# Optimization experiments

Hardware: AMD Instinct MI355X
Metric: run time of the kernel (lower is better)

Reference implementation:

```python
import jax, jax.numpy as jnp
import numpy as np

T, K, H, I, E = 8192, 2, 1024, 2816, 8


def setup_inputs() -> dict:
    key = jax.random.key(0)
    k1, k2, k3, k4, k5 = jax.random.split(key, 5)
    hidden_states = jax.random.normal(k1, (T, H), dtype=jnp.float32)
    expert_routing_table = jax.random.randint(k2, (T, K), 0, E)
    router_weights = jax.random.uniform(k3, (T, K), dtype=jnp.float32)
    # permuted_weights=True: weights stored so forward is x @ w
    # w13: fused gate+up proj [E, H, 2I]; w2: down proj [E, I, H]
    w13 = jax.random.normal(k4, (E, H, 2 * I), dtype=jnp.float32) * (1.0 / np.sqrt(H))
    w2 = jax.random.normal(k5, (E, I, H), dtype=jnp.float32) * (1.0 / np.sqrt(I))
    return {
        "hidden_states": hidden_states,
        "expert_routing_table": expert_routing_table,
        "router_weights": router_weights,
        "w13": w13,
        "w2": w2,
    }


def reference(hidden_states, expert_routing_table, router_weights, w13, w2):
    # Semantics of hpu.mixture_of_experts with activation='silu':
    # out[t] = sum_k rw[t,k] * ( (silu(x@w1g[e]) * (x@w1u[e])) @ w2[e] ), e = table[t,k]
    n_experts = w13.shape[0]
    inter = w2.shape[1]
    # per-token combine coefficient for each expert: [T, E]
    onehot = jax.nn.one_hot(expert_routing_table, n_experts, dtype=hidden_states.dtype)  # [T,K,E]
    coeff = jnp.einsum("tke,tk->te", onehot, router_weights)
    out = jnp.zeros_like(hidden_states)
    for e in range(n_experts):
        gu = hidden_states @ w13[e]            # [T, 2I]
        gate, up = gu[:, :inter], gu[:, inter:]
        h = jax.nn.silu(gate) * up             # [T, I]
        out = out + coeff[:, e:e + 1] * (h @ w2[e])
    return out
```

## Files before the change

kernel.cpp:

```cpp
#include <hip/hip_runtime.h>

typedef unsigned short u16;
typedef unsigned int u32;
typedef __bf16 bf16x8 __attribute__((ext_vector_type(8)));
typedef float f32x4 __attribute__((ext_vector_type(4)));
typedef u16 u16x4 __attribute__((ext_vector_type(4)));
typedef u16 u16x8 __attribute__((ext_vector_type(8)));

#define T_TOK 8192
#define HDIM 1024
#define IDIM 2816
#define NEXP 8
#define NPAIR (T_TOK * 2)
#define MAXRB 71

#define XB_OFF   (147456u)
#define W13T_OFF (XB_OFF + 16777216u)
#define W2T_OFF  (W13T_OFF + 92274688u)
#define H_OFF    (W2T_OFF + 46137344u)
#define WS_NEED  ((size_t)H_OFF + 102367232u)

__device__ __forceinline__ u16 f2bf(float f) {
  u32 u = __builtin_bit_cast(u32, f);
  u32 r = u + 0x7fffu + ((u >> 16) & 1u);
  return (u16)(r >> 16);
}

#define GLD16(g, l) __builtin_amdgcn_global_load_lds( \
    (const __attribute__((address_space(1))) void*)(g), \
    (__attribute__((address_space(3))) void*)(l), 16, 0, 0)

#define WAITVM(N) asm volatile("s_waitcnt vmcnt(" #N ")" ::: "memory")

__device__ __forceinline__ void pbar() {
  __builtin_amdgcn_sched_barrier(0);
  asm volatile("" ::: "memory");
  __builtin_amdgcn_s_barrier();
  asm volatile("" ::: "memory");
  __builtin_amdgcn_sched_barrier(0);
}

__global__ void init_meta(int* meta) {
  if (threadIdx.x < 16) meta[threadIdx.x] = 0;
}

__global__ void count_k(const int* __restrict__ routing, int* __restrict__ meta) {
  int i = blockIdx.x * 256 + threadIdx.x;
  if (i < NPAIR) atomicAdd(&meta[routing[i]], 1);
}

__global__ void scan_k(int* __restrict__ meta) {
  if (threadIdx.x == 0) {
    int rb = 0;
    for (int e = 0; e < NEXP; ++e) {
      meta[16 + e] = rb * 256;
      int nrb = (meta[e] + 255) >> 8;
      for (int i = 0; i < nrb; ++i) meta[32 + rb + i] = e;
      rb += nrb;
    }
    meta[24] = rb;
  }
}

__global__ void fill_pairs(int* __restrict__ pairs) {
  pairs[blockIdx.x * 256 + threadIdx.x] = -1;
}

__global__ void scatter_k(const int* __restrict__ routing, int* __restrict__ meta,
                          int* __restrict__ pairs, int* __restrict__ inv) {
  int i = blockIdx.x * 256 + threadIdx.x;
  if (i < NPAIR) {
    int e = routing[i];
    int pos = atomicAdd(&meta[8 + e], 1);
    int row = meta[16 + e] + pos;
    pairs[row] = i;
    inv[i] = row;
  }
}

__global__ void conv_x(const float* __restrict__ in, u16* __restrict__ out) {
  int i = blockIdx.x * 256 + threadIdx.x;
  float4 a = ((const float4*)in)[2 * i];
  float4 b = ((const float4*)in)[2 * i + 1];
  u16x8 o = { f2bf(a.x), f2bf(a.y), f2bf(a.z), f2bf(a.w),
              f2bf(b.x), f2bf(b.y), f2bf(b.z), f2bf(b.w) };
  ((u16x8*)out)[i] = o;
}

#define TSW(r, c) (((((c) >> 2) ^ ((((r) >> 4) & 3) << 2)) << 2) | ((c) & 3))
__global__ void transpose_cvt(const float* __restrict__ in, u16* __restrict__ out,
                              int R, int C) {
  __shared__ float tile[64][68];
  size_t base = (size_t)blockIdx.z * (size_t)R * (size_t)C;
  in += base; out += base;
  int t = threadIdx.x;
  int r0 = blockIdx.y * 64, c0 = blockIdx.x * 64;
  int lr = t >> 4, cb = t & 15;
#pragma unroll
  for (int p = 0; p < 4; ++p) {
    int row = p * 16 + lr;
    float4 v = *(const float4*)&in[(size_t)(r0 + row) * C + c0 + cb * 4];
    int pc = ((cb ^ ((p & 3) << 2)) << 2);
    tile[row][pc] = v.x; tile[row][pc + 1] = v.y;
    tile[row][pc + 2] = v.z; tile[row][pc + 3] = v.w;
  }
  __syncthreads();
  int oc = t >> 2, g0 = (t & 3) * 2;
#pragma unroll
  for (int gg = 0; gg < 2; ++gg) {
    int g = g0 + gg;
    u16x8 o = { f2bf(tile[g * 8 + 0][TSW(g * 8 + 0, oc)]), f2bf(tile[g * 8 + 1][TSW(g * 8 + 1, oc)]),
                f2bf(tile[g * 8 + 2][TSW(g * 8 + 2, oc)]), f2bf(tile[g * 8 + 3][TSW(g * 8 + 3, oc)]),
                f2bf(tile[g * 8 + 4][TSW(g * 8 + 4, oc)]), f2bf(tile[g * 8 + 5][TSW(g * 8 + 5, oc)]),
                f2bf(tile[g * 8 + 6][TSW(g * 8 + 6, oc)]), f2bf(tile[g * 8 + 7][TSW(g * 8 + 7, oc)]) };
    *(u16x8*)&out[(size_t)(c0 + oc) * R + r0 + g * 8] = o;
  }
}

__global__ __launch_bounds__(512, 2) void gemm1_k(
    const u16* __restrict__ Xb, const u16* __restrict__ W13T,
    const int* __restrict__ pairs, const int* __restrict__ meta,
    const float* __restrict__ rwf, u16* __restrict__ Hb) {
  int lin = blockIdx.x + 22 * blockIdx.y;
  int xcd = lin & 7, slot = lin >> 3;
  int flat = (xcd < 2) ? xcd * 196 + slot : 392 + (xcd - 2) * 195 + slot;
  int bx = flat / 71, rb = flat % 71;
  if (rb >= meta[24]) return;
  const int e = meta[32 + rb];
  const int bn0 = bx * 128;
  const int tid = threadIdx.x, lane = tid & 63, w = tid >> 6;
  const int wr = w >> 2, wc = w & 3;
  const int rowBase = rb * 256;

  __shared__ __align__(16) u16 lds[65536];
  char* const lb = (char*)lds;

  const int tr = tid >> 3;
  const int swk = ((tid & 7) << 4) ^ ((tr & 7) << 4);
  const u16* aS[4]; const u16* bS[4];
  const u16* wBase = W13T + (size_t)e * (2 * IDIM) * HDIM;
#pragma unroll
  for (int s = 0; s < 4; ++s) {
    int pr = pairs[rowBase + s * 64 + tr];
    int tok = pr < 0 ? 0 : (pr >> 1);
    aS[s] = Xb + (size_t)tok * HDIM + (swk >> 1);
    bS[s] = wBase + (size_t)((tr >> 5) * IDIM + bn0 + s * 32 + (tr & 31)) * HDIM + (swk >> 1);
  }

#define STGA(b, h, kt) { GLD16(aS[(h)*2]   + (kt)*64, lb + (b)*32768 + (h)*16384 + tid*16); \
                         GLD16(aS[(h)*2+1] + (kt)*64, lb + (b)*32768 + (h)*16384 + 8192 + tid*16); }
#define STGB(b, h, kt) { GLD16(bS[(h)*2]   + (kt)*64, lb + 65536 + (b)*32768 + (h)*16384 + tid*16); \
                         GLD16(bS[(h)*2+1] + (kt)*64, lb + 65536 + (b)*32768 + (h)*16384 + 8192 + tid*16); }

  const int l15 = lane & 15, l4 = lane >> 4, l7 = lane & 7;
  const int ko0 = (l4 * 16) ^ (l7 << 4);
  const int ko1 = (64 + l4 * 16) ^ (l7 << 4);
  const int aFB = wr * 16384 + l15 * 128;
  const int bFB = 65536 + (wc * 64 + l15) * 128;

#define LDA(d, b, mh, mf, ko) d = *(const bf16x8*)(lb + (b)*32768 + aFB + (mh)*8192 + (mf)*2048 + (ko))
#define LDB(d, b, nf, ko)     d = *(const bf16x8*)(lb + (b)*32768 + bFB + (nf)*2048 + (ko))

#define MFQ(mh, A, B) \
  _Pragma("unroll") for (int mf = 0; mf < 4; ++mf) \
  _Pragma("unroll") for (int nf = 0; nf < 4; ++nf) \
    acc[(mh)*4+mf][nf] = __builtin_amdgcn_mfma_f32_16x16x32_bf16(A[mf], B[nf], acc[(mh)*4+mf][nf], 0, 0, 0);

  f32x4 acc[8][4];
  const f32x4 fz = {0.f, 0.f, 0.f, 0.f};
#pragma unroll
  for (int i = 0; i < 8; ++i)
#pragma unroll
    for (int j = 0; j < 4; ++j) acc[i][j] = fz;

  STGB(0, 0, 0); STGB(0, 1, 0); STGA(0, 0, 0); STGA(0, 1, 0); STGB(1, 0, 1); STGB(1, 1, 1);
  WAITVM(4);
  pbar();

  bf16x8 aF[4], b0F[4], b1F[4];
#define ITER1(b, t1, t2) { \
     \
    _Pragma("unroll") for (int f = 0; f < 4; ++f) { LDA(aF[f], b, 0, f, ko0); LDB(b0F[f], b, f, ko0); } \
    STGA((b)^1, 0, t1); \
    pbar(); \
    __builtin_amdgcn_s_setprio(1); MFQ(0, aF, b0F); __builtin_amdgcn_s_setprio(0); \
    pbar(); \
     \
    _Pragma("unroll") for (int f = 0; f < 4; ++f) { LDA(aF[f], b, 0, f, ko1); LDB(b1F[f], b, f, ko1); } \
    STGA((b)^1, 1, t1); \
    pbar(); \
    __builtin_amdgcn_s_setprio(1); MFQ(0, aF, b1F); __builtin_amdgcn_s_setprio(0); \
    pbar(); \
     \
    _Pragma("unroll") for (int f = 0; f < 4; ++f) { LDA(aF[f], b, 1, f, ko0); } \
    STGB(b, 0, t2); \
    pbar(); \
    __builtin_amdgcn_s_setprio(1); MFQ(1, aF, b0F); __builtin_amdgcn_s_setprio(0); \
    pbar(); \
     \
    _Pragma("unroll") for (int f = 0; f < 4; ++f) { LDA(aF[f], b, 1, f, ko1); } \
    STGB(b, 1, t2); \
    pbar(); \
    __builtin_amdgcn_s_setprio(1); MFQ(1, aF, b1F); __builtin_amdgcn_s_setprio(0); \
    WAITVM(4); \
    pbar(); \
  }

  for (int jj = 0; jj < 8; ++jj) {
    const int ta = (2 * jj + 1) & 15, tb = (2 * jj + 2) & 15, tc = (2 * jj + 3) & 15;
    ITER1(0, ta, tb);
    ITER1(1, tb, tc);
  }
#undef ITER1
#undef STGA
#undef STGB
#undef LDA
#undef LDB
#undef MFQ

  const int ct = l4;
#pragma unroll
  for (int mf = 0; mf < 8; ++mf) {
#pragma unroll
    for (int j = 0; j < 4; ++j) {
      int m = wr * 128 + mf * 16 + ct * 4 + j;
      int pr = rowBase + m;
      int pair = pairs[pr];
      float rw = pair >= 0 ? rwf[pair] : 0.f;
      u16* hrow = Hb + (size_t)pr * IDIM + bn0 + wc * 32 + l15;
#pragma unroll
      for (int g = 0; g < 2; ++g) {
        float gv = acc[mf][g][j], uv = acc[mf][g + 2][j];
        float s = gv / (1.f + __expf(-gv));
        hrow[g * 16] = f2bf(s * uv * rw);
      }
    }
  }
}

__global__ __launch_bounds__(256, 2) void gemm2_k(
    const u16* __restrict__ Hb, const u16* __restrict__ W2T,
    const int* __restrict__ meta, float* __restrict__ part) {
  int lin = blockIdx.y + 142 * blockIdx.x;
  int xcd = lin & 7, slot = lin >> 3;
  int flat = xcd * 142 + slot;
  int bx = flat / 142, rb2 = flat % 142;
  if (rb2 >= meta[24] * 2) return;
  const int e = meta[32 + (rb2 >> 1)];
  const int bn0 = bx * 128;
  const int tid = threadIdx.x, lane = tid & 63, w = tid >> 6;
  const int wr = w >> 1, wc = w & 1;
  const int rowBase = rb2 * 128;

  __shared__ __align__(16) u16 lds2[32768];
  char* const lb = (char*)lds2;

  const int sr = tid >> 3;
  const int swk = ((tid & 7) << 4) ^ ((sr & 7) << 4);
  const u16* aS[4]; const u16* bS[4];
#pragma unroll
  for (int j = 0; j < 4; ++j) {
    aS[j] = Hb + (size_t)(rowBase + j * 32 + sr) * IDIM + (swk >> 1);
    bS[j] = W2T + (size_t)e * HDIM * IDIM + (size_t)(bn0 + j * 32 + sr) * IDIM + (swk >> 1);
  }

#define STG_A2(b, kt) { GLD16(aS[0] + (kt)*64, lb + (b)*16384 + tid*16); \
                        GLD16(aS[1] + (kt)*64, lb + (b)*16384 + 4096 + tid*16); \
                        GLD16(aS[2] + (kt)*64, lb + (b)*16384 + 8192 + tid*16); \
                        GLD16(aS[3] + (kt)*64, lb + (b)*16384 + 12288 + tid*16); }
#define STG_B2(b, kt) { GLD16(bS[0] + (kt)*64, lb + 32768 + (b)*16384 + tid*16); \
                        GLD16(bS[1] + (kt)*64, lb + 32768 + (b)*16384 + 4096 + tid*16); \
                        GLD16(bS[2] + (kt)*64, lb + 32768 + (b)*16384 + 8192 + tid*16); \
                        GLD16(bS[3] + (kt)*64, lb + 32768 + (b)*16384 + 12288 + tid*16); }

  const int l15 = lane & 15, l4 = lane >> 4, l7 = lane & 7;
  const int ko0 = (l4 * 16) ^ (l7 << 4);
  const int ko1 = (64 + l4 * 16) ^ (l7 << 4);
  const int aFB = (wr * 64 + l15) * 128;
  const int bFB = (wc * 64 + l15) * 128;

#define LDAF2(d, b, mf, ko) d = *(const bf16x8*)(lb + (b)*16384 + aFB + (mf)*2048 + (ko))
#define LDBF2(d, b, nf, ko) d = *(const bf16x8*)(lb + 32768 + (b)*16384 + bFB + (nf)*2048 + (ko))

#define MF16v(A, B) \
  _Pragma("unroll") for (int mf = 0; mf < 4; ++mf) \
  _Pragma("unroll") for (int nf = 0; nf < 4; ++nf) \
    acc[mf][nf] = __builtin_amdgcn_mfma_f32_16x16x32_bf16(A[mf], B[nf], acc[mf][nf], 0, 0, 0);

  f32x4 acc[4][4];
  const f32x4 fz = {0.f, 0.f, 0.f, 0.f};
#pragma unroll
  for (int i = 0; i < 4; ++i)
#pragma unroll
    for (int j = 0; j < 4; ++j) acc[i][j] = fz;

  STG_A2(0, 0); STG_B2(0, 0); STG_A2(1, 1);
  WAITVM(4);
  pbar();

  bf16x8 a0[4], a1[4], b0[4], b1[4];
  for (int i = 0; i < 22; ++i) {
    const int t1 = 2 * i + 1;
    const int nt0 = (2 * i + 2 < 44) ? 2 * i + 2 : 0;
    const int nt1 = (2 * i + 3 < 44) ? 2 * i + 3 : 0;
#pragma unroll
    for (int f = 0; f < 4; ++f) { LDAF2(a0[f], 0, f, ko0); LDAF2(a1[f], 0, f, ko1);
                                  LDBF2(b0[f], 0, f, ko0); LDBF2(b1[f], 0, f, ko1); }
    STG_B2(1, t1);
    pbar();
    __builtin_amdgcn_s_setprio(1); MF16v(a0, b0); __builtin_amdgcn_s_setprio(0);
    pbar();
    STG_A2(0, nt0);
    pbar();
    __builtin_amdgcn_s_setprio(1); MF16v(a1, b1); __builtin_amdgcn_s_setprio(0);
    WAITVM(4);
    pbar();
#pragma unroll
    for (int f = 0; f < 4; ++f) { LDAF2(a0[f], 1, f, ko0); LDAF2(a1[f], 1, f, ko1);
                                  LDBF2(b0[f], 1, f, ko0); LDBF2(b1[f], 1, f, ko1); }
    STG_B2(0, nt0);
    pbar();
    __builtin_amdgcn_s_setprio(1); MF16v(a0, b0); __builtin_amdgcn_s_setprio(0);
    pbar();
    STG_A2(1, nt1);
    pbar();
    __builtin_amdgcn_s_setprio(1); MF16v(a1, b1); __builtin_amdgcn_s_setprio(0);
    WAITVM(4);
    pbar();
  }
#undef STG_A2
#undef STG_B2
#undef LDAF2
#undef LDBF2
#undef MF16v

  WAITVM(0);
  const int ct = l4;
#pragma unroll
  for (int mf = 0; mf < 4; ++mf) {
#pragma unroll
    for (int j = 0; j < 4; ++j) {
      int m = rowBase + wr * 64 + mf * 16 + ct * 4 + j;
      float* prow = part + (size_t)m * HDIM + bn0 + wc * 64 + l15;
#pragma unroll
      for (int nf = 0; nf < 4; ++nf) prow[nf * 16] = acc[mf][nf][j];
    }
  }
}

__global__ void reduce_k(const float* __restrict__ part, const int* __restrict__ inv,
                         float* __restrict__ out) {
  int t = blockIdx.x;
  int c = threadIdx.x * 4;
  int r0 = inv[2 * t], r1 = inv[2 * t + 1];
  float4 a = *(const float4*)&part[(size_t)r0 * HDIM + c];
  float4 b = *(const float4*)&part[(size_t)r1 * HDIM + c];
  float4 o = { a.x + b.x, a.y + b.y, a.z + b.z, a.w + b.w };
  *(float4*)&out[(size_t)t * HDIM + c] = o;
}

extern "C" void kernel_launch(void* const* d_in, const int* in_sizes, int n_in,
                              void* d_out, int out_size, void* d_ws, size_t ws_size,
                              hipStream_t stream) {
  const float* X = (const float*)d_in[0];
  const int* routing = (const int*)d_in[1];
  const float* rwf = (const float*)d_in[2];
  const float* w13 = (const float*)d_in[3];
  const float* w2 = (const float*)d_in[4];
  float* out = (float*)d_out;
  char* ws = (char*)d_ws;

  if (ws_size < WS_NEED) {
    hipMemsetAsync(d_out, 0, (size_t)T_TOK * HDIM * sizeof(float), stream);
    return;
  }

  int* meta = (int*)ws;
  int* pairs = (int*)(ws + 1024);
  int* inv = (int*)(ws + 73728);
  u16* Xb = (u16*)(ws + XB_OFF);
  u16* W13T = (u16*)(ws + W13T_OFF);
  u16* W2T = (u16*)(ws + W2T_OFF);
  u16* Hb = (u16*)(ws + H_OFF);
  float* part = (float*)(ws + W13T_OFF);

  init_meta<<<1, 64, 0, stream>>>(meta);
  count_k<<<NPAIR / 256, 256, 0, stream>>>(routing, meta);
  scan_k<<<1, 64, 0, stream>>>(meta);
  fill_pairs<<<MAXRB, 256, 0, stream>>>(pairs);
  scatter_k<<<NPAIR / 256, 256, 0, stream>>>(routing, meta, pairs, inv);
  conv_x<<<(T_TOK * HDIM / 8) / 256, 256, 0, stream>>>(X, Xb);
  transpose_cvt<<<dim3(5632 / 64, 1024 / 64, NEXP), 256, 0, stream>>>(w13, W13T, 1024, 5632);
  transpose_cvt<<<dim3(1024 / 64, 2816 / 64, NEXP), 256, 0, stream>>>(w2, W2T, 2816, 1024);
  gemm1_k<<<dim3(22, MAXRB), 512, 0, stream>>>(Xb, W13T, pairs, meta, rwf, Hb);
  gemm2_k<<<dim3(8, 2 * MAXRB), 256, 0, stream>>>(Hb, W2T, meta, part);
  reduce_k<<<T_TOK, 256, 0, stream>>>(part, inv, out);
}
```

Baseline: 579.8 us.

## Switch GEMMs to 32x32 MFMA, retile gemm2 with split-K and bf16 partials

Measured after the change: 631.2 us. 8.9% more time.

```diff
diff --git a/kernel.cpp b/kernel.cpp
--- a/kernel.cpp
+++ b/kernel.cpp
@@ -3,8 +3,7 @@
 typedef unsigned short u16;
 typedef unsigned int u32;
 typedef __bf16 bf16x8 __attribute__((ext_vector_type(8)));
-typedef float f32x4 __attribute__((ext_vector_type(4)));
-typedef u16 u16x4 __attribute__((ext_vector_type(4)));
+typedef float f32x16 __attribute__((ext_vector_type(16)));
 typedef u16 u16x8 __attribute__((ext_vector_type(8)));
 
 #define T_TOK 8192
@@ -13,6 +12,8 @@
 #define NEXP 8
 #define NPAIR (T_TOK * 2)
 #define MAXRB 71
+#define PADROWS (MAXRB * 256)
+#define PARTSZ ((size_t)PADROWS * HDIM)
 
 #define XB_OFF   (147456u)
 #define W13T_OFF (XB_OFF + 16777216u)
@@ -24,6 +25,10 @@
   u32 u = __builtin_bit_cast(u32, f);
   u32 r = u + 0x7fffu + ((u >> 16) & 1u);
   return (u16)(r >> 16);
+}
+__device__ __forceinline__ float bf2f(u16 v) {
+  u32 u = ((u32)v) << 16;
+  return __builtin_bit_cast(float, u);
 }
 
 #define GLD16(g, l) __builtin_amdgcn_global_load_lds( \
@@ -40,8 +45,9 @@
   __builtin_amdgcn_sched_barrier(0);
 }
 
-__global__ void init_meta(int* meta) {
-  if (threadIdx.x < 16) meta[threadIdx.x] = 0;
+__global__ void fillinit_k(int* __restrict__ pairs, int* __restrict__ meta) {
+  if (blockIdx.x == 0 && threadIdx.x < 16) meta[threadIdx.x] = 0;
+  pairs[blockIdx.x * 256 + threadIdx.x] = -1;
 }
 
 __global__ void count_k(const int* __restrict__ routing, int* __restrict__ meta) {
@@ -60,10 +66,6 @@
     }
     meta[24] = rb;
   }
-}
-
-__global__ void fill_pairs(int* __restrict__ pairs) {
-  pairs[blockIdx.x * 256 + threadIdx.x] = -1;
 }
 
 __global__ void scatter_k(const int* __restrict__ routing, int* __restrict__ meta,
@@ -152,56 +154,61 @@
 #define STGB(b, h, kt) { GLD16(bS[(h)*2]   + (kt)*64, lb + 65536 + (b)*32768 + (h)*16384 + tid*16); \
                          GLD16(bS[(h)*2+1] + (kt)*64, lb + 65536 + (b)*32768 + (h)*16384 + 8192 + tid*16); }
 
-  const int l15 = lane & 15, l4 = lane >> 4, l7 = lane & 7;
-  const int ko0 = (l4 * 16) ^ (l7 << 4);
-  const int ko1 = (64 + l4 * 16) ^ (l7 << 4);
-  const int aFB = wr * 16384 + l15 * 128;
-  const int bFB = 65536 + (wc * 64 + l15) * 128;
-
-#define LDA(d, b, mh, mf, ko) d = *(const bf16x8*)(lb + (b)*32768 + aFB + (mh)*8192 + (mf)*2048 + (ko))
-#define LDB(d, b, nf, ko)     d = *(const bf16x8*)(lb + (b)*32768 + bFB + (nf)*2048 + (ko))
-
-#define MFQ(mh, A, B) \
-  _Pragma("unroll") for (int mf = 0; mf < 4; ++mf) \
-  _Pragma("unroll") for (int nf = 0; nf < 4; ++nf) \
-    acc[(mh)*4+mf][nf] = __builtin_amdgcn_mfma_f32_16x16x32_bf16(A[mf], B[nf], acc[(mh)*4+mf][nf], 0, 0, 0);
-
-  f32x4 acc[8][4];
-  const f32x4 fz = {0.f, 0.f, 0.f, 0.f};
-#pragma unroll
-  for (int i = 0; i < 8; ++i)
-#pragma unroll
-    for (int j = 0; j < 4; ++j) acc[i][j] = fz;
+  const int cl = lane & 31, hi = lane >> 5, swr = (lane & 7) << 4;
+  const int hi16 = hi * 16;
+  const int ko0 = (0  + hi16) ^ swr;
+  const int ko1 = (32 + hi16) ^ swr;
+  const int ko2 = (64 + hi16) ^ swr;
+  const int ko3 = (96 + hi16) ^ swr;
+  const int aFB = wr * 16384 + cl * 128;
+  const int bFB = 65536 + wc * 8192 + cl * 128;
+
+#define LDA(d, b, mfi, K) d = *(const bf16x8*)(lb + (b)*32768 + aFB + (mfi)*4096 + ko##K)
+#define LDB(d, b, nf, K)  d = *(const bf16x8*)(lb + (b)*32768 + bFB + (nf)*4096 + ko##K)
+
+#define MF32(mq, A, BV) \
+  _Pragma("unroll") for (int mf2 = 0; mf2 < 2; ++mf2) \
+  _Pragma("unroll") for (int nf = 0; nf < 2; ++nf) \
+  _Pragma("unroll") for (int ki = 0; ki < 2; ++ki) \
+    acc[(mq)*2+mf2][nf] = __builtin_amdgcn_mfma_f32_32x32x16_bf16(A[mf2*2+ki], BV[nf*2+ki], acc[(mq)*2+mf2][nf], 0, 0, 0);
+
+  f32x16 acc[4][2];
+#pragma unroll
+  for (int i = 0; i < 4; ++i)
+#pragma unroll
+    for (int j = 0; j < 2; ++j) acc[i][j] = (f32x16)0.f;
 
   STGB(0, 0, 0); STGB(0, 1, 0); STGA(0, 0, 0); STGA(0, 1, 0); STGB(1, 0, 1); STGB(1, 1, 1);
   WAITVM(4);
   pbar();
 
-  bf16x8 aF[4], b0F[4], b1F[4];
+  bf16x8 aF[4], bK0[4], bK1[4];
 #define ITER1(b, t1, t2) { \
      \
-    _Pragma("unroll") for (int f = 0; f < 4; ++f) { LDA(aF[f], b, 0, f, ko0); LDB(b0F[f], b, f, ko0); } \
+    LDA(aF[0], b, 0, 0); LDA(aF[1], b, 0, 1); LDA(aF[2], b, 1, 0); LDA(aF[3], b, 1, 1); \
+    LDB(bK0[0], b, 0, 0); LDB(bK0[1], b, 0, 1); LDB(bK0[2], b, 1, 0); LDB(bK0[3], b, 1, 1); \
     STGA((b)^1, 0, t1); \
     pbar(); \
-    __builtin_amdgcn_s_setprio(1); MFQ(0, aF, b0F); __builtin_amdgcn_s_setprio(0); \
+    __builtin_amdgcn_s_setprio(1); MF32(0, aF, bK0); __builtin_amdgcn_s_setprio(0); \
     pbar(); \
      \
-    _Pragma("unroll") for (int f = 0; f < 4; ++f) { LDA(aF[f], b, 0, f, ko1); LDB(b1F[f], b, f, ko1); } \
+    LDA(aF[0], b, 0, 2); LDA(aF[1], b, 0, 3); LDA(aF[2], b, 1, 2); LDA(aF[3], b, 1, 3); \
+    LDB(bK1[0], b, 0, 2); LDB(bK1[1], b, 0, 3); LDB(bK1[2], b, 1, 2); LDB(bK1[3], b, 1, 3); \
     STGA((b)^1, 1, t1); \
     pbar(); \
-    __builtin_amdgcn_s_setprio(1); MFQ(0, aF, b1F); __builtin_amdgcn_s_setprio(0); \
+    __builtin_amdgcn_s_setprio(1); MF32(0, aF, bK1); __builtin_amdgcn_s_setprio(0); \
     pbar(); \
      \
-    _Pragma("unroll") for (int f = 0; f < 4; ++f) { LDA(aF[f], b, 1, f, ko0); } \
+    LDA(aF[0], b, 2, 0); LDA(aF[1], b, 2, 1); LDA(aF[2], b, 3, 0); LDA(aF[3], b, 3, 1); \
     STGB(b, 0, t2); \
     pbar(); \
-    __builtin_amdgcn_s_setprio(1); MFQ(1, aF, b0F); __builtin_amdgcn_s_setprio(0); \
+    __builtin_amdgcn_s_setprio(1); MF32(1, aF, bK0); __builtin_amdgcn_s_setprio(0); \
     pbar(); \
      \
-    _Pragma("unroll") for (int f = 0; f < 4; ++f) { LDA(aF[f], b, 1, f, ko1); } \
+    LDA(aF[0], b, 2, 2); LDA(aF[1], b, 2, 3); LDA(aF[2], b, 3, 2); LDA(aF[3], b, 3, 3); \
     STGB(b, 1, t2); \
     pbar(); \
-    __builtin_amdgcn_s_setprio(1); MFQ(1, aF, b1F); __builtin_amdgcn_s_setprio(0); \
+    __builtin_amdgcn_s_setprio(1); MF32(1, aF, bK1); __builtin_amdgcn_s_setprio(0); \
     WAITVM(4); \
     pbar(); \
   }
@@ -216,147 +223,151 @@
 #undef STGB
 #undef LDA
 #undef LDB
-#undef MFQ
-
-  const int ct = l4;
-#pragma unroll
-  for (int mf = 0; mf < 8; ++mf) {
-#pragma unroll
-    for (int j = 0; j < 4; ++j) {
-      int m = wr * 128 + mf * 16 + ct * 4 + j;
+
+#pragma unroll
+  for (int mf = 0; mf < 4; ++mf) {
+#pragma unroll
+    for (int reg = 0; reg < 16; ++reg) {
+      int m = wr * 128 + mf * 32 + (reg & 3) + 8 * (reg >> 2) + 4 * hi;
       int pr = rowBase + m;
       int pair = pairs[pr];
       float rw = pair >= 0 ? rwf[pair] : 0.f;
-      u16* hrow = Hb + (size_t)pr * IDIM + bn0 + wc * 32 + l15;
-#pragma unroll
-      for (int g = 0; g < 2; ++g) {
-        float gv = acc[mf][g][j], uv = acc[mf][g + 2][j];
-        float s = gv / (1.f + __expf(-gv));
-        hrow[g * 16] = f2bf(s * uv * rw);
-      }
+      float gv = acc[mf][0][reg], uv = acc[mf][1][reg];
+      float s = gv / (1.f + __expf(-gv));
+      Hb[(size_t)pr * IDIM + bn0 + wc * 32 + cl] = f2bf(s * uv * rw);
     }
   }
 }
 
-__global__ __launch_bounds__(256, 2) void gemm2_k(
+__global__ __launch_bounds__(512, 2) void gemm2_k(
     const u16* __restrict__ Hb, const u16* __restrict__ W2T,
-    const int* __restrict__ meta, float* __restrict__ part) {
-  int lin = blockIdx.y + 142 * blockIdx.x;
+    const int* __restrict__ meta, u16* __restrict__ part) {
+  int lin = blockIdx.x + 4 * blockIdx.y + 284 * blockIdx.z;
   int xcd = lin & 7, slot = lin >> 3;
-  int flat = xcd * 142 + slot;
-  int bx = flat / 142, rb2 = flat % 142;
-  if (rb2 >= meta[24] * 2) return;
-  const int e = meta[32 + (rb2 >> 1)];
-  const int bn0 = bx * 128;
+  int flat = xcd * 71 + slot;
+  int kz = flat / 284, rm = flat % 284;
+  int bx = rm / 71, rb = rm % 71;
+  if (rb >= meta[24]) return;
+  const int e = meta[32 + rb];
+  const int bn0 = bx * 256;
+  const int kz0 = kz * 1408;
   const int tid = threadIdx.x, lane = tid & 63, w = tid >> 6;
-  const int wr = w >> 1, wc = w & 1;
-  const int rowBase = rb2 * 128;
-
-  __shared__ __align__(16) u16 lds2[32768];
-  char* const lb = (char*)lds2;
-
-  const int sr = tid >> 3;
-  const int swk = ((tid & 7) << 4) ^ ((sr & 7) << 4);
+  const int wr = w >> 2, wc = w & 3;
+  const int rowBase = rb * 256;
+
+  __shared__ __align__(16) u16 lds[65536];
+  char* const lb = (char*)lds;
+
+  const int tr = tid >> 3;
+  const int swk = ((tid & 7) << 4) ^ ((tr & 7) << 4);
   const u16* aS[4]; const u16* bS[4];
-#pragma unroll
-  for (int j = 0; j < 4; ++j) {
-    aS[j] = Hb + (size_t)(rowBase + j * 32 + sr) * IDIM + (swk >> 1);
-    bS[j] = W2T + (size_t)e * HDIM * IDIM + (size_t)(bn0 + j * 32 + sr) * IDIM + (swk >> 1);
-  }
-
-#define STG_A2(b, kt) { GLD16(aS[0] + (kt)*64, lb + (b)*16384 + tid*16); \
-                        GLD16(aS[1] + (kt)*64, lb + (b)*16384 + 4096 + tid*16); \
-                        GLD16(aS[2] + (kt)*64, lb + (b)*16384 + 8192 + tid*16); \
-                        GLD16(aS[3] + (kt)*64, lb + (b)*16384 + 12288 + tid*16); }
-#define STG_B2(b, kt) { GLD16(bS[0] + (kt)*64, lb + 32768 + (b)*16384 + tid*16); \
-                        GLD16(bS[1] + (kt)*64, lb + 32768 + (b)*16384 + 4096 + tid*16); \
-                        GLD16(bS[2] + (kt)*64, lb + 32768 + (b)*16384 + 8192 + tid*16); \
-                        GLD16(bS[3] + (kt)*64, lb + 32768 + (b)*16384 + 12288 + tid*16); }
-
-  const int l15 = lane & 15, l4 = lane >> 4, l7 = lane & 7;
-  const int ko0 = (l4 * 16) ^ (l7 << 4);
-  const int ko1 = (64 + l4 * 16) ^ (l7 << 4);
-  const int aFB = (wr * 64 + l15) * 128;
-  const int bFB = (wc * 64 + l15) * 128;
-
-#define LDAF2(d, b, mf, ko) d = *(const bf16x8*)(lb + (b)*16384 + aFB + (mf)*2048 + (ko))
-#define LDBF2(d, b, nf, ko) d = *(const bf16x8*)(lb + 32768 + (b)*16384 + bFB + (nf)*2048 + (ko))
-
-#define MF16v(A, B) \
-  _Pragma("unroll") for (int mf = 0; mf < 4; ++mf) \
-  _Pragma("unroll") for (int nf = 0; nf < 4; ++nf) \
-    acc[mf][nf] = __builtin_amdgcn_mfma_f32_16x16x32_bf16(A[mf], B[nf], acc[mf][nf], 0, 0, 0);
-
-  f32x4 acc[4][4];
-  const f32x4 fz = {0.f, 0.f, 0.f, 0.f};
+  const u16* w2Base = W2T + (size_t)e * HDIM * IDIM;
+#pragma unroll
+  for (int s = 0; s < 4; ++s) {
+    aS[s] = Hb + (size_t)(rowBase + s * 64 + tr) * IDIM + kz0 + (swk >> 1);
+    bS[s] = w2Base + (size_t)(bn0 + s * 64 + tr) * IDIM + kz0 + (swk >> 1);
+  }
+
+#define STGA(b, h, kt) { GLD16(aS[(h)*2]   + (kt)*64, lb + (b)*32768 + (h)*16384 + tid*16); \
+                         GLD16(aS[(h)*2+1] + (kt)*64, lb + (b)*32768 + (h)*16384 + 8192 + tid*16); }
+#define STGB(b, h, kt) { GLD16(bS[(h)*2]   + (kt)*64, lb + 65536 + (b)*32768 + (h)*16384 + tid*16); \
+                         GLD16(bS[(h)*2+1] + (kt)*64, lb + 65536 + (b)*32768 + (h)*16384 + 8192 + tid*16); }
+
+  const int cl = lane & 31, hi = lane >> 5, swr = (lane & 7) << 4;
+  const int hi16 = hi * 16;
+  const int ko0 = (0  + hi16) ^ swr;
+  const int ko1 = (32 + hi16) ^ swr;
+  const int ko2 = (64 + hi16) ^ swr;
+  const int ko3 = (96 + hi16) ^ swr;
+  const int aFB = wr * 16384 + cl * 128;
+  const int bFB = 65536 + wc * 8192 + cl * 128;
+
+#define LDA(d, b, mfi, K) d = *(const bf16x8*)(lb + (b)*32768 + aFB + (mfi)*4096 + ko##K)
+#define LDB(d, b, nf, K)  d = *(const bf16x8*)(lb + (b)*32768 + bFB + (nf)*4096 + ko##K)
+
+  f32x16 acc[4][2];
 #pragma unroll
   for (int i = 0; i < 4; ++i)
 #pragma unroll
-    for (int j = 0; j < 4; ++j) acc[i][j] = fz;
-
-  STG_A2(0, 0); STG_B2(0, 0); STG_A2(1, 1);
+    for (int j = 0; j < 2; ++j) acc[i][j] = (f32x16)0.f;
+
+  STGB(0, 0, 0); STGB(0, 1, 0); STGA(0, 0, 0); STGA(0, 1, 0); STGB(1, 0, 1); STGB(1, 1, 1);
   WAITVM(4);
   pbar();
 
-  bf16x8 a0[4], a1[4], b0[4], b1[4];
-  for (int i = 0; i < 22; ++i) {
-    const int t1 = 2 * i + 1;
-    const int nt0 = (2 * i + 2 < 44) ? 2 * i + 2 : 0;
-    const int nt1 = (2 * i + 3 < 44) ? 2 * i + 3 : 0;
-#pragma unroll
-    for (int f = 0; f < 4; ++f) { LDAF2(a0[f], 0, f, ko0); LDAF2(a1[f], 0, f, ko1);
-                                  LDBF2(b0[f], 0, f, ko0); LDBF2(b1[f], 0, f, ko1); }
-    STG_B2(1, t1);
-    pbar();
-    __builtin_amdgcn_s_setprio(1); MF16v(a0, b0); __builtin_amdgcn_s_setprio(0);
-    pbar();
-    STG_A2(0, nt0);
-    pbar();
-    __builtin_amdgcn_s_setprio(1); MF16v(a1, b1); __builtin_amdgcn_s_setprio(0);
-    WAITVM(4);
-    pbar();
-#pragma unroll
-    for (int f = 0; f < 4; ++f) { LDAF2(a0[f], 1, f, ko0); LDAF2(a1[f], 1, f, ko1);
-                                  LDBF2(b0[f], 1, f, ko0); LDBF2(b1[f], 1, f, ko1); }
-    STG_B2(0, nt0);
-    pbar();
-    __builtin_amdgcn_s_setprio(1); MF16v(a0, b0); __builtin_amdgcn_s_setprio(0);
-    pbar();
-    STG_A2(1, nt1);
-    pbar();
-    __builtin_amdgcn_s_setprio(1); MF16v(a1, b1); __builtin_amdgcn_s_setprio(0);
-    WAITVM(4);
-    pbar();
-  }
-#undef STG_A2
-#undef STG_B2
-#undef LDAF2
-#undef LDBF2
-#undef MF16v
-
-  WAITVM(0);
-  const int ct = l4;
+  bf16x8 aF[4], bK0[4], bK1[4];
+#define ITER2(b, t1, t2) { \
+    LDA(aF[0], b, 0, 0); LDA(aF[1], b, 0, 1); LDA(aF[2], b, 1, 0); LDA(aF[3], b, 1, 1); \
+    LDB(bK0[0], b, 0, 0); LDB(bK0[1], b, 0, 1); LDB(bK0[2], b, 1, 0); LDB(bK0[3], b, 1, 1); \
+    STGA((b)^1, 0, t1); \
+    pbar(); \
+    __builtin_amdgcn_s_setprio(1); MF32(0, aF, bK0); __builtin_amdgcn_s_setprio(0); \
+    pbar(); \
+    LDA(aF[0], b, 0, 2); LDA(aF[1], b, 0, 3); LDA(aF[2], b, 1, 2); LDA(aF[3], b, 1, 3); \
+    LDB(bK1[0], b, 0, 2); LDB(bK1[1], b, 0, 3); LDB(bK1[2], b, 1, 2); LDB(bK1[3], b, 1, 3); \
+    STGA((b)^1, 1, t1); \
+    pbar(); \
+    __builtin_amdgcn_s_setprio(1); MF32(0, aF, bK1); __builtin_amdgcn_s_setprio(0); \
+    pbar(); \
+    LDA(aF[0], b, 2, 0); LDA(aF[1], b, 2, 1); LDA(aF[2], b, 3, 0); LDA(aF[3], b, 3, 1); \
+    STGB(b, 0, t2); \
+    pbar(); \
+    __builtin_amdgcn_s_setprio(1); MF32(1, aF, bK0); __builtin_amdgcn_s_setprio(0); \
+    pbar(); \
+    LDA(aF[0], b, 2, 2); LDA(aF[1], b, 2, 3); LDA(aF[2], b, 3, 2); LDA(aF[3], b, 3, 3); \
+    STGB(b, 1, t2); \
+    pbar(); \
+    __builtin_amdgcn_s_setprio(1); MF32(1, aF, bK1); __builtin_amdgcn_s_setprio(0); \
+    WAITVM(4); \
+    pbar(); \
+  }
+
+  for (int jj = 0; jj < 11; ++jj) {
+    const int t1 = 2 * jj + 1;
+    const int tb = (2 * jj + 2 < 22) ? 2 * jj + 2 : 0;
+    const int tc = (2 * jj + 3 < 22) ? 2 * jj + 3 : 0;
+    ITER2(0, t1, tb);
+    ITER2(1, tb, tc);
+  }
+#undef ITER2
+#undef STGA
+#undef STGB
+#undef LDA
+#undef LDB
+
+  u16* pz = part + (size_t)kz * PARTSZ;
 #pragma unroll
   for (int mf = 0; mf < 4; ++mf) {
 #pragma unroll
-    for (int j = 0; j < 4; ++j) {
-      int m = rowBase + wr * 64 + mf * 16 + ct * 4 + j;
-      float* prow = part + (size_t)m * HDIM + bn0 + wc * 64 + l15;
-#pragma unroll
-      for (int nf = 0; nf < 4; ++nf) prow[nf * 16] = acc[mf][nf][j];
+    for (int reg = 0; reg < 16; ++reg) {
+      int m = rowBase + wr * 128 + mf * 32 + (reg & 3) + 8 * (reg >> 2) + 4 * hi;
+      u16* prow = pz + (size_t)m * HDIM + bn0 + wc * 64 + cl;
+      prow[0]  = f2bf(acc[mf][0][reg]);
+      prow[32] = f2bf(acc[mf][1][reg]);
     }
   }
 }
 
-__global__ void reduce_k(const float* __restrict__ part, const int* __restrict__ inv,
+__global__ void reduce_k(const u16* __restrict__ part, const int* __restrict__ inv,
                          float* __restrict__ out) {
   int t = blockIdx.x;
-  int c = threadIdx.x * 4;
+  int c = threadIdx.x * 8;
   int r0 = inv[2 * t], r1 = inv[2 * t + 1];
-  float4 a = *(const float4*)&part[(size_t)r0 * HDIM + c];
-  float4 b = *(const float4*)&part[(size_t)r1 * HDIM + c];
-  float4 o = { a.x + b.x, a.y + b.y, a.z + b.z, a.w + b.w };
-  *(float4*)&out[(size_t)t * HDIM + c] = o;
+  u16x8 a0 = *(const u16x8*)&part[(size_t)r0 * HDIM + c];
+  u16x8 a1 = *(const u16x8*)&part[(size_t)r1 * HDIM + c];
+  u16x8 b0 = *(const u16x8*)&part[PARTSZ + (size_t)r0 * HDIM + c];
+  u16x8 b1 = *(const u16x8*)&part[PARTSZ + (size_t)r1 * HDIM + c];
+  float4 o0, o1;
+  o0.x = bf2f(a0[0]) + bf2f(a1[0]) + bf2f(b0[0]) + bf2f(b1[0]);
+  o0.y = bf2f(a0[1]) + bf2f(a1[1]) + bf2f(b0[1]) + bf2f(b1[1]);
+  o0.z = bf2f(a0[2]) + bf2f(a1[2]) + bf2f(b0[2]) + bf2f(b1[2]);
+  o0.w = bf2f(a0[3]) + bf2f(a1[3]) + bf2f(b0[3]) + bf2f(b1[3]);
+  o1.x = bf2f(a0[4]) + bf2f(a1[4]) + bf2f(b0[4]) + bf2f(b1[4]);
+  o1.y = bf2f(a0[5]) + bf2f(a1[5]) + bf2f(b0[5]) + bf2f(b1[5]);
+  o1.z = bf2f(a0[6]) + bf2f(a1[6]) + bf2f(b0[6]) + bf2f(b1[6]);
+  o1.w = bf2f(a0[7]) + bf2f(a1[7]) + bf2f(b0[7]) + bf2f(b1[7]);
+  *(float4*)&out[(size_t)t * HDIM + c] = o0;
+  *(float4*)&out[(size_t)t * HDIM + c + 4] = o1;
 }
 
 extern "C" void kernel_launch(void* const* d_in, const int* in_sizes, int n_in,
@@ -382,17 +393,16 @@
   u16* W13T = (u16*)(ws + W13T_OFF);
   u16* W2T = (u16*)(ws + W2T_OFF);
   u16* Hb = (u16*)(ws + H_OFF);
-  float* part = (float*)(ws + W13T_OFF);
-
-  init_meta<<<1, 64, 0, stream>>>(meta);
+  u16* part = (u16*)(ws + W13T_OFF);
+
+  fillinit_k<<<MAXRB, 256, 0, stream>>>(pairs, meta);
   count_k<<<NPAIR / 256, 256, 0, stream>>>(routing, meta);
   scan_k<<<1, 64, 0, stream>>>(meta);
-  fill_pairs<<<MAXRB, 256, 0, stream>>>(pairs);
   scatter_k<<<NPAIR / 256, 256, 0, stream>>>(routing, meta, pairs, inv);
   conv_x<<<(T_TOK * HDIM / 8) / 256, 256, 0, stream>>>(X, Xb);
   transpose_cvt<<<dim3(5632 / 64, 1024 / 64, NEXP), 256, 0, stream>>>(w13, W13T, 1024, 5632);
   transpose_cvt<<<dim3(1024 / 64, 2816 / 64, NEXP), 256, 0, stream>>>(w2, W2T, 2816, 1024);
   gemm1_k<<<dim3(22, MAXRB), 512, 0, stream>>>(Xb, W13T, pairs, meta, rwf, Hb);
-  gemm2_k<<<dim3(8, 2 * MAXRB), 256, 0, stream>>>(Hb, W2T, meta, part);
-  reduce_k<<<T_TOK, 256, 0, stream>>>(part, inv, out);
-}
+  gemm2_k<<<dim3(4, MAXRB, 2), 512, 0, stream>>>(Hb, W2T, meta, part);
+  reduce_k<<<T_TOK, 128, 0, stream>>>(part, inv, out);
+}
```

## Software-pipeline LDS fragment loads in gemm1 and merge init kernels

Applied to the files above, without the earlier changes.

New measurement: 575.8 us. No clear change (-0.7%).

```diff
diff --git a/kernel.cpp b/kernel.cpp
--- a/kernel.cpp
+++ b/kernel.cpp
@@ -4,7 +4,6 @@
 typedef unsigned int u32;
 typedef __bf16 bf16x8 __attribute__((ext_vector_type(8)));
 typedef float f32x4 __attribute__((ext_vector_type(4)));
-typedef u16 u16x4 __attribute__((ext_vector_type(4)));
 typedef u16 u16x8 __attribute__((ext_vector_type(8)));
 
 #define T_TOK 8192
@@ -40,8 +39,9 @@
   __builtin_amdgcn_sched_barrier(0);
 }
 
-__global__ void init_meta(int* meta) {
-  if (threadIdx.x < 16) meta[threadIdx.x] = 0;
+__global__ void fillinit_k(int* __restrict__ pairs, int* __restrict__ meta) {
+  if (blockIdx.x == 0 && threadIdx.x < 16) meta[threadIdx.x] = 0;
+  pairs[blockIdx.x * 256 + threadIdx.x] = -1;
 }
 
 __global__ void count_k(const int* __restrict__ routing, int* __restrict__ meta) {
@@ -60,10 +60,6 @@
     }
     meta[24] = rb;
   }
-}
-
-__global__ void fill_pairs(int* __restrict__ pairs) {
-  pairs[blockIdx.x * 256 + threadIdx.x] = -1;
 }
 
 __global__ void scatter_k(const int* __restrict__ routing, int* __restrict__ meta,
@@ -177,41 +173,44 @@
   WAITVM(4);
   pbar();
 
-  bf16x8 aF[4], b0F[4], b1F[4];
-#define ITER1(b, t1, t2) { \
+  bf16x8 aA[4], aB[4], bK0[4], bK1[4];
+#pragma unroll
+  for (int f = 0; f < 4; ++f) { LDA(aA[f], 0, 0, f, ko0); LDB(bK0[f], 0, f, ko0); }
+
+#define TILE1(b, t1, t2) { \
      \
-    _Pragma("unroll") for (int f = 0; f < 4; ++f) { LDA(aF[f], b, 0, f, ko0); LDB(b0F[f], b, f, ko0); } \
+    _Pragma("unroll") for (int f = 0; f < 4; ++f) { LDA(aB[f], b, 0, f, ko1); LDB(bK1[f], b, f, ko1); } \
     STGA((b)^1, 0, t1); \
     pbar(); \
-    __builtin_amdgcn_s_setprio(1); MFQ(0, aF, b0F); __builtin_amdgcn_s_setprio(0); \
+    __builtin_amdgcn_s_setprio(1); MFQ(0, aA, bK0); __builtin_amdgcn_s_setprio(0); \
     pbar(); \
      \
-    _Pragma("unroll") for (int f = 0; f < 4; ++f) { LDA(aF[f], b, 0, f, ko1); LDB(b1F[f], b, f, ko1); } \
+    _Pragma("unroll") for (int f = 0; f < 4; ++f) { LDA(aA[f], b, 1, f, ko0); } \
     STGA((b)^1, 1, t1); \
     pbar(); \
-    __builtin_amdgcn_s_setprio(1); MFQ(0, aF, b1F); __builtin_amdgcn_s_setprio(0); \
+    __builtin_amdgcn_s_setprio(1); MFQ(0, aB, bK1); __builtin_amdgcn_s_setprio(0); \
     pbar(); \
      \
-    _Pragma("unroll") for (int f = 0; f < 4; ++f) { LDA(aF[f], b, 1, f, ko0); } \
+    _Pragma("unroll") for (int f = 0; f < 4; ++f) { LDA(aB[f], b, 1, f, ko1); } \
     STGB(b, 0, t2); \
     pbar(); \
-    __builtin_amdgcn_s_setprio(1); MFQ(1, aF, b0F); __builtin_amdgcn_s_setprio(0); \
+    __builtin_amdgcn_s_setprio(1); MFQ(1, aA, bK0); __builtin_amdgcn_s_setprio(0); \
     pbar(); \
      \
-    _Pragma("unroll") for (int f = 0; f < 4; ++f) { LDA(aF[f], b, 1, f, ko1); } \
+    WAITVM(2); \
+    _Pragma("unroll") for (int f = 0; f < 4; ++f) { LDA(aA[f], (b)^1, 0, f, ko0); LDB(bK0[f], (b)^1, f, ko0); } \
     STGB(b, 1, t2); \
     pbar(); \
-    __builtin_amdgcn_s_setprio(1); MFQ(1, aF, b1F); __builtin_amdgcn_s_setprio(0); \
-    WAITVM(4); \
+    __builtin_amdgcn_s_setprio(1); MFQ(1, aB, bK1); __builtin_amdgcn_s_setprio(0); \
     pbar(); \
   }
 
   for (int jj = 0; jj < 8; ++jj) {
     const int ta = (2 * jj + 1) & 15, tb = (2 * jj + 2) & 15, tc = (2 * jj + 3) & 15;
-    ITER1(0, ta, tb);
-    ITER1(1, tb, tc);
-  }
-#undef ITER1
+    TILE1(0, ta, tb);
+    TILE1(1, tb, tc);
+  }
+#undef TILE1
 #undef STGA
 #undef STGB
 #undef LDA
@@ -384,10 +383,9 @@
   u16* Hb = (u16*)(ws + H_OFF);
   float* part = (float*)(ws + W13T_OFF);
 
-  init_meta<<<1, 64, 0, stream>>>(meta);
+  fillinit_k<<<MAXRB, 256, 0, stream>>>(pairs, meta);
   count_k<<<NPAIR / 256, 256, 0, stream>>>(routing, meta);
   scan_k<<<1, 64, 0, stream>>>(meta);
-  fill_pairs<<<MAXRB, 256, 0, stream>>>(pairs);
   scatter_k<<<NPAIR / 256, 256, 0, stream>>>(routing, meta, pairs, inv);
   conv_x<<<(T_TOK * HDIM / 8) / 256, 256, 0, stream>>>(X, Xb);
   transpose_cvt<<<dim3(5632 / 64, 1024 / 64, NEXP), 256, 0, stream>>>(w13, W13T, 1024, 5632);
```
